# Kernel tuning notes

Hardware: AMD Instinct MI355X
Metric: run time of the kernel (lower is better)

## Reference

```python
import jax, jax.numpy as jnp
import numpy as np
import math

B, S, D, H = 8, 1024, 512, 8  # batch, seqlen, d_model, heads
DK = D // H

def setup_inputs() -> dict:
    key = jax.random.key(0)
    ks = jax.random.split(key, 8)
    std = 1.0 / math.sqrt(D)
    return {
        "x": jax.random.normal(ks[0], (B, S, D), jnp.float32),
        "utT_similarities": jax.random.uniform(ks[1], (B, S, S), jnp.float32),
        "Wk": jax.random.normal(ks[2], (D, D), jnp.float32) * std,
        "bk": jnp.zeros((D,), jnp.float32),
        "Wv": jax.random.normal(ks[3], (D, D), jnp.float32) * std,
        "bv": jnp.zeros((D,), jnp.float32),
        "Wo": jax.random.normal(ks[4], (D, D), jnp.float32) * std,
        "bo": jnp.zeros((D,), jnp.float32),
        "gammas": jax.random.normal(ks[5], (H, 1, 1), jnp.float32) * 0.1,
    }

def reference(x, utT_similarities, Wk, bk, Wv, bv, Wo, bo, gammas):
    b, s, d = x.shape
    h = gammas.shape[0]
    dk = d // h
    NEG = -1e32

    def split_heads(t):  # [b,s,d] -> [b,h,s,dk]
        return t.reshape(b, s, h, dk).transpose(0, 2, 1, 3)

    # kq_same=True: q and k share k_linear
    q = split_heads(x @ Wk.T + bk)
    k = q
    v = split_heads(x @ Wv.T + bv)

    scores = jnp.einsum('bhid,bhjd->bhij', q, k) / jnp.sqrt(jnp.float32(dk))
    scores = scores * utT_similarities[:, None, :, :]

    mask = jnp.tril(jnp.ones((s, s), dtype=bool))  # causal, incl diagonal (mask=1)

    # distance-decay block (no_grad in torch -> stop_gradient)
    s_ = jax.nn.softmax(jnp.where(mask, scores, NEG), axis=-1) * mask
    distcum = jnp.cumsum(s_, axis=-1)
    disttotal = jnp.sum(s_, axis=-1, keepdims=True)
    idx = jnp.arange(s)
    position_effect = jnp.abs(idx[None, :] - idx[:, None]).astype(jnp.float32)  # [s,s]
    dist_scores = jnp.sqrt(jnp.clip((disttotal - distcum) * position_effect, 0.0, None))
    dist_scores = jax.lax.stop_gradient(dist_scores)

    gamma = -jax.nn.softplus(gammas)[None]  # [1,h,1,1]
    total_effect = jnp.clip(jnp.exp(dist_scores * gamma), 1e-5, 1e5)

    scores = jax.nn.softmax(jnp.where(mask, scores * total_effect, NEG), axis=-1)
    # zero_pad=False (mask=1 path), dropout is identity in eval
    out = jnp.einsum('bhij,bhjd->bhid', scores, v)
    out = out.transpose(0, 2, 1, 3).reshape(b, s, d)
    return out @ Wo.T + bo
```

## Files before the change

### kernel.cpp

```cpp
#include <hip/hip_runtime.h>
#include <math.h>

#define NB   8
#define SS   1024
#define DD   512
#define HH   8
#define DKK  64
#define NEGF (-3.0e38f)

#define QSTR 88
#define SSTR 257
#define PSTR 280

typedef _Float16 half8 __attribute__((ext_vector_type(8)));
typedef float    f32x4 __attribute__((ext_vector_type(4)));

#define GLDS16(g, l) __builtin_amdgcn_global_load_lds( \
    (const __attribute__((address_space(1))) void*)(g), \
    (__attribute__((address_space(3))) void*)(l), 16, 0, 0)

__global__ __launch_bounds__(256) void cvt_fp16(
    const float* __restrict__ x,  _Float16* __restrict__ xh,
    const float* __restrict__ wk, _Float16* __restrict__ wkh,
    const float* __restrict__ wv, _Float16* __restrict__ wvh,
    const float* __restrict__ wo, _Float16* __restrict__ woh)
{
    const size_t NX = (size_t)NB * SS * DD;
    const size_t NW = (size_t)DD * DD;
    size_t f = ((size_t)blockIdx.x * 256 + threadIdx.x) * 8;
    const float* src; _Float16* dst; size_t off;
    if (f < NX)               { src = x;  dst = xh;  off = f; }
    else if (f < NX + NW)     { src = wk; dst = wkh; off = f - NX; }
    else if (f < NX + 2*NW)   { src = wv; dst = wvh; off = f - NX - 2*NW + NW; }
    else                      { src = wo; dst = woh; off = f - NX - 2*NW; }
    float4 f0 = *(const float4*)&src[off];
    float4 f1 = *(const float4*)&src[off + 4];
    half8 hv = {(_Float16)f0.x,(_Float16)f0.y,(_Float16)f0.z,(_Float16)f0.w,
                (_Float16)f1.x,(_Float16)f1.y,(_Float16)f1.z,(_Float16)f1.w};
    *(half8*)&dst[off] = hv;
}

__global__ __launch_bounds__(256) void gemm_qv(
    const _Float16* __restrict__ xh,
    const _Float16* __restrict__ wkh, const float* __restrict__ bk,
    const _Float16* __restrict__ wvh, const float* __restrict__ bv,
    _Float16* __restrict__ q_ws, _Float16* __restrict__ vt_ws)
{
    __shared__ __align__(16) _Float16 Ah[128 * 32];
    __shared__ __align__(16) _Float16 Bh[128 * 32];

    const int m0  = blockIdx.x * 128;
    const int n0c = blockIdx.y * 128;
    const bool is_v = (n0c >= DD);
    const _Float16* __restrict__ Wp = is_v ? wvh : wkh;
    const float*    __restrict__ bp = is_v ? bv : bk;
    const int n0 = n0c & (DD - 1);

    const int tid  = threadIdx.x;
    const int w    = tid >> 6;
    const int lane = tid & 63;
    const int quad = lane >> 4;
    const int n    = lane & 15;
    const int wm   = w >> 1, wn = w & 1;

    const int ci0 = (w * 2 + 0) * 64 + lane;
    const int ci1 = (w * 2 + 1) * 64 + lane;
    const int r0c = ci0 >> 2, c0c = (ci0 & 3) * 8;
    const int r1c = ci1 >> 2, c1c = (ci1 & 3) * 8;
    _Float16* ldsA0 = &Ah[(w * 2 + 0) * 512];
    _Float16* ldsA1 = &Ah[(w * 2 + 1) * 512];
    _Float16* ldsB0 = &Bh[(w * 2 + 0) * 512];
    _Float16* ldsB1 = &Bh[(w * 2 + 1) * 512];

    f32x4 acc[4][4] = {};

    for (int k0 = 0; k0 < DD; k0 += 32) {
        __syncthreads();
        GLDS16(&xh[(size_t)(m0 + r0c) * DD + k0 + c0c], ldsA0);
        GLDS16(&xh[(size_t)(m0 + r1c) * DD + k0 + c1c], ldsA1);
        GLDS16(&Wp[(size_t)(n0 + r0c) * DD + k0 + c0c], ldsB0);
        GLDS16(&Wp[(size_t)(n0 + r1c) * DD + k0 + c1c], ldsB1);
        __syncthreads();
        half8 af[4], bf[4];
        #pragma unroll
        for (int mi = 0; mi < 4; ++mi)
            af[mi] = *(const half8*)&Ah[(wm*64 + mi*16 + n) * 32 + quad*8];
        #pragma unroll
        for (int ni = 0; ni < 4; ++ni)
            bf[ni] = *(const half8*)&Bh[(wn*64 + ni*16 + n) * 32 + quad*8];
        #pragma unroll
        for (int mi = 0; mi < 4; ++mi)
            #pragma unroll
            for (int ni = 0; ni < 4; ++ni)
                acc[mi][ni] = __builtin_amdgcn_mfma_f32_16x16x32_f16(
                    af[mi], bf[ni], acc[mi][ni], 0, 0, 0);
    }

    #pragma unroll
    for (int mi = 0; mi < 4; ++mi) {
        #pragma unroll
        for (int ni = 0; ni < 4; ++ni) {
            const int col = n0 + wn*64 + ni*16 + n;
            const int h   = col >> 6;
            const int dk  = col & 63;
            const float bias = bp[col];
            const int gbase = m0 + wm*64 + mi*16 + quad*4;
            const int bidx  = gbase >> 10;
            const int sr    = gbase & (SS - 1);
            if (!is_v) {
                #pragma unroll
                for (int reg = 0; reg < 4; ++reg)
                    q_ws[((size_t)(bidx * HH + h) * SS + sr + reg) * DKK + dk] =
                        (_Float16)(acc[mi][ni][reg] + bias);
            } else {
                _Float16 h4[4];
                #pragma unroll
                for (int reg = 0; reg < 4; ++reg)
                    h4[reg] = (_Float16)(acc[mi][ni][reg] + bias);
                *(uint2*)&vt_ws[((size_t)(bidx * HH + h) * DKK + dk) * SS + sr] =
                    *(uint2*)h4;
            }
        }
    }
}

__global__ __launch_bounds__(256) void gemm_out(
    const _Float16* __restrict__ A,
    const _Float16* __restrict__ woh, const float* __restrict__ bo,
    float* __restrict__ out)
{
    __shared__ __align__(16) _Float16 Ah[128 * 32];
    __shared__ __align__(16) _Float16 Bh[128 * 32];

    const int m0 = blockIdx.x * 128;
    const int n0 = blockIdx.y * 128;

    const int tid  = threadIdx.x;
    const int w    = tid >> 6;
    const int lane = tid & 63;
    const int quad = lane >> 4;
    const int n    = lane & 15;
    const int wm   = w >> 1, wn = w & 1;

    const int ci0 = (w * 2 + 0) * 64 + lane;
    const int ci1 = (w * 2 + 1) * 64 + lane;
    const int r0c = ci0 >> 2, c0c = (ci0 & 3) * 8;
    const int r1c = ci1 >> 2, c1c = (ci1 & 3) * 8;
    _Float16* ldsA0 = &Ah[(w * 2 + 0) * 512];
    _Float16* ldsA1 = &Ah[(w * 2 + 1) * 512];
    _Float16* ldsB0 = &Bh[(w * 2 + 0) * 512];
    _Float16* ldsB1 = &Bh[(w * 2 + 1) * 512];

    f32x4 acc[4][4] = {};

    for (int k0 = 0; k0 < DD; k0 += 32) {
        __syncthreads();
        GLDS16(&A[(size_t)(m0 + r0c) * DD + k0 + c0c], ldsA0);
        GLDS16(&A[(size_t)(m0 + r1c) * DD + k0 + c1c], ldsA1);
        GLDS16(&woh[(size_t)(n0 + r0c) * DD + k0 + c0c], ldsB0);
        GLDS16(&woh[(size_t)(n0 + r1c) * DD + k0 + c1c], ldsB1);
        __syncthreads();
        half8 af[4], bf[4];
        #pragma unroll
        for (int mi = 0; mi < 4; ++mi)
            af[mi] = *(const half8*)&Ah[(wm*64 + mi*16 + n) * 32 + quad*8];
        #pragma unroll
        for (int ni = 0; ni < 4; ++ni)
            bf[ni] = *(const half8*)&Bh[(wn*64 + ni*16 + n) * 32 + quad*8];
        #pragma unroll
        for (int mi = 0; mi < 4; ++mi)
            #pragma unroll
            for (int ni = 0; ni < 4; ++ni)
                acc[mi][ni] = __builtin_amdgcn_mfma_f32_16x16x32_f16(
                    af[mi], bf[ni], acc[mi][ni], 0, 0, 0);
    }

    #pragma unroll
    for (int mi = 0; mi < 4; ++mi) {
        #pragma unroll
        for (int ni = 0; ni < 4; ++ni) {
            const int col  = n0 + wn*64 + ni*16 + n;
            const float bias = bo[col];
            const int gbase = m0 + wm*64 + mi*16 + quad*4;
            #pragma unroll
            for (int reg = 0; reg < 4; ++reg)
                out[(size_t)(gbase + reg) * DD + col] = acc[mi][ni][reg] + bias;
        }
    }
}

__global__ __launch_bounds__(1024) void attn_mfma(
    const _Float16* __restrict__ q,
    const _Float16* __restrict__ vt,
    const float* __restrict__ utT,
    const float* __restrict__ gammas,
    _Float16* __restrict__ attn)
{
    __shared__ __align__(16) float    s_lds[2 * 16 * SSTR];
    __shared__ __align__(16) _Float16 q_lds[16 * QSTR];
    _Float16* p_lds = (_Float16*)s_lds;

    const int tid  = threadIdx.x;
    const int w    = tid >> 6;
    const int lane = tid & 63;
    const int quad = lane >> 4;
    const int n    = lane & 15;
    const int bh   = blockIdx.y;
    const int b    = bh >> 3;
    const int h    = bh & 7;
    const int r0   = blockIdx.x * 16;

    const _Float16* __restrict__ kq  = q  + (size_t)bh * SS * DKK;
    const _Float16* __restrict__ vtp = vt + (size_t)bh * DKK * SS;

    const int nchunk = (r0 + 16 + 255) >> 8;
    const int nt     = nchunk * 4;

    if (tid < 256) {
        const int row = tid >> 4;
        const int c   = tid & 15;
        *(uint2*)&q_lds[row * QSTR + c * 4] =
            *(const uint2*)&kq[(size_t)(r0 + row) * DKK + c * 4];
    }
    __syncthreads();

    float sreg[16];
    #pragma unroll
    for (int t2 = 0; t2 < 16; ++t2) sreg[t2] = NEGF;

    #pragma unroll
    for (int c0 = 0; c0 < 4; ++c0) {
        if (c0 < nchunk) {
            const int j0  = c0 * 256;
            const int buf = (c0 & 1) * 16 * SSTR;
            const int jbase = j0 + w * 16;
            if (jbase <= r0 + 15) {
                const _Float16* krow = &kq[(size_t)(jbase + n) * DKK];
                half8 b0 = *(const half8*)&krow[quad * 8];
                half8 b1 = *(const half8*)&krow[32 + quad * 8];
                half8 a0 = *(const half8*)&q_lds[n * QSTR + quad * 8];
                half8 a1 = *(const half8*)&q_lds[n * QSTR + 32 + quad * 8];
                f32x4 d = {0.f, 0.f, 0.f, 0.f};
                d = __builtin_amdgcn_mfma_f32_16x16x32_f16(a0, b0, d, 0, 0, 0);
                d = __builtin_amdgcn_mfma_f32_16x16x32_f16(a1, b1, d, 0, 0, 0);
                const int j = jbase + n;
                #pragma unroll
                for (int reg = 0; reg < 4; ++reg) {
                    const int i = r0 + quad * 4 + reg;
                    float val = NEGF;
                    if (j <= i)
                        val = d[reg] * 0.125f * utT[((size_t)b * SS + i) * SS + j];
                    s_lds[buf + (quad * 4 + reg) * SSTR + w * 16 + n] = val;
                }
            } else {
                #pragma unroll
                for (int reg = 0; reg < 4; ++reg)
                    s_lds[buf + (quad * 4 + reg) * SSTR + w * 16 + n] = NEGF;
            }
            __syncthreads();
            #pragma unroll
            for (int ttl = 0; ttl < 4; ++ttl)
                sreg[c0 * 4 + ttl] = s_lds[buf + w * SSTR + ttl * 64 + lane];
        }
    }

    const int i_row = r0 + w;

    float m1 = NEGF;
    #pragma unroll
    for (int t2 = 0; t2 < 16; ++t2) if (t2 < nt) m1 = fmaxf(m1, sreg[t2]);
    #pragma unroll
    for (int o = 32; o >= 1; o >>= 1) m1 = fmaxf(m1, __shfl_xor(m1, o));

    float ee[16];
    float z1 = 0.f;
    #pragma unroll
    for (int t2 = 0; t2 < 16; ++t2) {
        float e = 0.f;
        if (t2 < nt) {
            const int j = t2 * 64 + lane;
            if (j <= i_row) e = __expf(sreg[t2] - m1);
        }
        ee[t2] = e;
        z1 += e;
    }
    #pragma unroll
    for (int o = 32; o >= 1; o >>= 1) z1 += __shfl_xor(z1, o);
    const float inv_z1 = 1.0f / z1;

    const float g     = gammas[h];
    const float gamma = -log1pf(__expf(g));

    float carry = 0.f;
    float m2 = NEGF;
    #pragma unroll
    for (int t2 = 0; t2 < 16; ++t2) {
        if (t2 < nt) {
            float xv = ee[t2];
            #pragma unroll
            for (int o = 1; o < 64; o <<= 1) {
                float y = __shfl_up(xv, (unsigned)o);
                if (lane >= o) xv += y;
            }
            const float tile_tot = __shfl(xv, 63);
            const float csum = (carry + xv) * inv_z1;
            carry += tile_tot;

            const int j = t2 * 64 + lane;
            const float pe = (float)(i_row - j);
            const float dd = fmaxf((1.0f - csum) * pe, 0.0f);
            float te = __expf(sqrtf(dd) * gamma);
            te = fminf(fmaxf(te, 1e-5f), 1e5f);
            const float nsv = (j <= i_row) ? sreg[t2] * te : NEGF;
            ee[t2] = nsv;
            m2 = fmaxf(m2, nsv);
        }
    }
    #pragma unroll
    for (int o = 32; o >= 1; o >>= 1) m2 = fmaxf(m2, __shfl_xor(m2, o));

    float z2 = 0.f;
    #pragma unroll
    for (int t2 = 0; t2 < 16; ++t2) {
        if (t2 < nt) {
            ee[t2] = __expf(ee[t2] - m2);
            z2 += ee[t2];
        }
    }
    #pragma unroll
    for (int o = 32; o >= 1; o >>= 1) z2 += __shfl_xor(z2, o);
    const float inv_z2 = 1.0f / z2;
    #pragma unroll
    for (int t2 = 0; t2 < 16; ++t2) if (t2 < nt) ee[t2] *= inv_z2;

    __syncthreads();

    f32x4 oacc = {0.f, 0.f, 0.f, 0.f};
    #pragma unroll
    for (int c0 = 0; c0 < 4; ++c0) {
        if (c0 < nchunk) {
            const int j0 = c0 * 256;
            const int pb = (c0 & 1) * 16 * PSTR;
            #pragma unroll
            for (int ttl = 0; ttl < 4; ++ttl)
                p_lds[pb + w * PSTR + ttl * 64 + lane] = (_Float16)ee[c0 * 4 + ttl];
            __syncthreads();
            if (w < 4) {
                int nkt = (r0 + 16 - j0 + 31) >> 5;
                nkt = (nkt > 8) ? 8 : nkt;
                const _Float16* vrow = &vtp[(size_t)(w * 16 + n) * SS + j0];
                for (int kt = 0; kt < nkt; ++kt) {
                    half8 a  = *(const half8*)&p_lds[pb + n * PSTR + kt * 32 + quad * 8];
                    half8 bb = *(const half8*)&vrow[kt * 32 + quad * 8];
                    oacc = __builtin_amdgcn_mfma_f32_16x16x32_f16(a, bb, oacc, 0, 0, 0);
                }
            }
        }
    }

    if (w < 4) {
        #pragma unroll
        for (int reg = 0; reg < 4; ++reg) {
            const int i = r0 + quad * 4 + reg;
            attn[(((size_t)b * SS + i) * HH + h) * DKK + w * 16 + n] =
                (_Float16)oacc[reg];
        }
    }
}

extern "C" void kernel_launch(void* const* d_in, const int* in_sizes, int n_in,
                              void* d_out, int out_size, void* d_ws, size_t ws_size,
                              hipStream_t stream) {
    const float* x      = (const float*)d_in[0];
    const float* utT    = (const float*)d_in[1];
    const float* Wk     = (const float*)d_in[2];
    const float* bk     = (const float*)d_in[3];
    const float* Wv     = (const float*)d_in[4];
    const float* bv     = (const float*)d_in[5];
    const float* Wo     = (const float*)d_in[6];
    const float* bo     = (const float*)d_in[7];
    const float* gammas = (const float*)d_in[8];
    float* out = (float*)d_out;

    const size_t NX  = (size_t)NB * SS * DD;
    const size_t NW  = (size_t)DD * DD;
    const size_t per = NX;

    _Float16* p      = (_Float16*)d_ws;
    _Float16* xh     = p;  p += NX;
    _Float16* wkh    = p;  p += NW;
    _Float16* wvh    = p;  p += NW;
    _Float16* woh    = p;  p += NW;
    _Float16* q_ws   = p;  p += per;
    _Float16* vt_ws  = p;  p += per;
    _Float16* attn_h = p;  p += per;

    const int cvt_blocks = (int)((NX + 3 * NW) / 8 / 256);
    cvt_fp16<<<cvt_blocks, dim3(256), 0, stream>>>(
        x, xh, Wk, wkh, Wv, wvh, Wo, woh);

    dim3 g1(64, 8);
    gemm_qv<<<g1, dim3(256), 0, stream>>>(xh, wkh, bk, wvh, bv, q_ws, vt_ws);

    dim3 g2(SS / 16, NB * HH);
    attn_mfma<<<g2, dim3(1024), 0, stream>>>(q_ws, vt_ws, utT, gammas, attn_h);

    dim3 g3(64, 4);
    gemm_out<<<g3, dim3(256), 0, stream>>>(attn_h, woh, bo, out);
}
```

Before: 330.1 us.

## Stage full score and probability rows in LDS to drop per-chunk barriers

The score tile is now sized to hold a whole 1024-column row for all 16 query rows, so each wave computes its QK^T tiles across the full key range before a single barrier, instead of looping over 256-column chunks with a barrier each. The PV stage likewise writes the full probability row to LDS once and runs one uninterrupted MFMA loop over all key tiles. The Q fragments are also hoisted out of the tile loop. This is meant to cut barrier count and loop overhead. In exchange the LDS footprint roughly doubles, which could reduce how many blocks fit per CU.

```diff
diff --git a/kernel.cpp b/kernel.cpp
--- a/kernel.cpp
+++ b/kernel.cpp
@@ -8,9 +8,9 @@
 #define DKK  64
 #define NEGF (-3.0e38f)
 
-#define QSTR 88
-#define SSTR 257
-#define PSTR 280
+#define QSTR  88
+#define SSTR2 1025
+#define PSTR2 1048
 
 typedef _Float16 half8 __attribute__((ext_vector_type(8)));
 typedef float    f32x4 __attribute__((ext_vector_type(4)));
@@ -196,7 +196,7 @@
     const float* __restrict__ gammas,
     _Float16* __restrict__ attn)
 {
-    __shared__ __align__(16) float    s_lds[2 * 16 * SSTR];
+    __shared__ __align__(16) float    s_lds[16 * SSTR2];
     __shared__ __align__(16) _Float16 q_lds[16 * QSTR];
     _Float16* p_lds = (_Float16*)s_lds;
 
@@ -224,22 +224,18 @@
     }
     __syncthreads();
 
-    float sreg[16];
-    #pragma unroll
-    for (int t2 = 0; t2 < 16; ++t2) sreg[t2] = NEGF;
-
-    #pragma unroll
-    for (int c0 = 0; c0 < 4; ++c0) {
-        if (c0 < nchunk) {
-            const int j0  = c0 * 256;
-            const int buf = (c0 & 1) * 16 * SSTR;
-            const int jbase = j0 + w * 16;
+    const half8 a0 = *(const half8*)&q_lds[n * QSTR + quad * 8];
+    const half8 a1 = *(const half8*)&q_lds[n * QSTR + 32 + quad * 8];
+
+    #pragma unroll
+    for (int k = 0; k < 4; ++k) {
+        const int jt = w + k * 16;
+        if (jt < nt * 4) {
+            const int jbase = jt * 16;
             if (jbase <= r0 + 15) {
                 const _Float16* krow = &kq[(size_t)(jbase + n) * DKK];
                 half8 b0 = *(const half8*)&krow[quad * 8];
                 half8 b1 = *(const half8*)&krow[32 + quad * 8];
-                half8 a0 = *(const half8*)&q_lds[n * QSTR + quad * 8];
-                half8 a1 = *(const half8*)&q_lds[n * QSTR + 32 + quad * 8];
                 f32x4 d = {0.f, 0.f, 0.f, 0.f};
                 d = __builtin_amdgcn_mfma_f32_16x16x32_f16(a0, b0, d, 0, 0, 0);
                 d = __builtin_amdgcn_mfma_f32_16x16x32_f16(a1, b1, d, 0, 0, 0);
@@ -250,19 +246,24 @@
                     float val = NEGF;
                     if (j <= i)
                         val = d[reg] * 0.125f * utT[((size_t)b * SS + i) * SS + j];
-                    s_lds[buf + (quad * 4 + reg) * SSTR + w * 16 + n] = val;
+                    s_lds[(quad * 4 + reg) * SSTR2 + jbase + n] = val;
                 }
             } else {
                 #pragma unroll
                 for (int reg = 0; reg < 4; ++reg)
-                    s_lds[buf + (quad * 4 + reg) * SSTR + w * 16 + n] = NEGF;
+                    s_lds[(quad * 4 + reg) * SSTR2 + jbase + n] = NEGF;
             }
-            __syncthreads();
-            #pragma unroll
-            for (int ttl = 0; ttl < 4; ++ttl)
-                sreg[c0 * 4 + ttl] = s_lds[buf + w * SSTR + ttl * 64 + lane];
-        }
-    }
+        }
+    }
+    __syncthreads();
+
+    float sreg[16];
+    #pragma unroll
+    for (int t2 = 0; t2 < 16; ++t2) sreg[t2] = NEGF;
+    #pragma unroll
+    for (int t2 = 0; t2 < 16; ++t2)
+        if (t2 < nt)
+            sreg[t2] = s_lds[w * SSTR2 + t2 * 64 + lane];
 
     const int i_row = r0 + w;
 
@@ -335,30 +336,21 @@
 
     __syncthreads();
 
-    f32x4 oacc = {0.f, 0.f, 0.f, 0.f};
-    #pragma unroll
-    for (int c0 = 0; c0 < 4; ++c0) {
-        if (c0 < nchunk) {
-            const int j0 = c0 * 256;
-            const int pb = (c0 & 1) * 16 * PSTR;
-            #pragma unroll
-            for (int ttl = 0; ttl < 4; ++ttl)
-                p_lds[pb + w * PSTR + ttl * 64 + lane] = (_Float16)ee[c0 * 4 + ttl];
-            __syncthreads();
-            if (w < 4) {
-                int nkt = (r0 + 16 - j0 + 31) >> 5;
-                nkt = (nkt > 8) ? 8 : nkt;
-                const _Float16* vrow = &vtp[(size_t)(w * 16 + n) * SS + j0];
-                for (int kt = 0; kt < nkt; ++kt) {
-                    half8 a  = *(const half8*)&p_lds[pb + n * PSTR + kt * 32 + quad * 8];
-                    half8 bb = *(const half8*)&vrow[kt * 32 + quad * 8];
-                    oacc = __builtin_amdgcn_mfma_f32_16x16x32_f16(a, bb, oacc, 0, 0, 0);
-                }
-            }
-        }
-    }
+    #pragma unroll
+    for (int t2 = 0; t2 < 16; ++t2)
+        if (t2 < nt)
+            p_lds[w * PSTR2 + t2 * 64 + lane] = (_Float16)ee[t2];
+    __syncthreads();
 
     if (w < 4) {
+        const int nkt = (r0 + 16 + 31) >> 5;
+        f32x4 oacc = {0.f, 0.f, 0.f, 0.f};
+        const _Float16* vrow = &vtp[(size_t)(w * 16 + n) * SS];
+        for (int kt = 0; kt < nkt; ++kt) {
+            half8 a  = *(const half8*)&p_lds[n * PSTR2 + kt * 32 + quad * 8];
+            half8 bb = *(const half8*)&vrow[kt * 32 + quad * 8];
+            oacc = __builtin_amdgcn_mfma_f32_16x16x32_f16(a, bb, oacc, 0, 0, 0);
+        }
         #pragma unroll
         for (int reg = 0; reg < 4; ++reg) {
             const int i = r0 + quad * 4 + reg;
```

New measurement: 402.3 us. +21.9%, slower.
